# Performance work log

Measured on AMD Instinct MI355X. Metric: run time of the kernel, lower is better.

Reference implementation:

```python
import jax, jax.numpy as jnp
import numpy as np
import math

D_MODEL = 1024
NHEAD = 16
FACTOR = 5


def setup_inputs() -> dict:
    key = jax.random.key(0)
    kq, kk, kv = jax.random.split(key, 3)
    B, L = 4, 2048
    Q = jax.random.normal(kq, (B, L, D_MODEL), dtype=jnp.float32)
    K = jax.random.normal(kk, (B, L, D_MODEL), dtype=jnp.float32)
    V = jax.random.normal(kv, (B, L, D_MODEL), dtype=jnp.float32)
    return {"Q": Q, "K": K, "V": V}


def reference(Q, K, V):
    B, q_len, _ = Q.shape
    k_len = K.shape[1]
    head_dim = D_MODEL // NHEAD
    scale = 1.0 / math.sqrt(head_dim)

    # [B, H, L, Dh]
    Qh = Q.reshape(B, q_len, NHEAD, head_dim).transpose(0, 2, 1, 3)
    Kh = K.reshape(B, k_len, NHEAD, head_dim).transpose(0, 2, 1, 3)
    Vh = V.reshape(B, k_len, NHEAD, head_dim).transpose(0, 2, 1, 3)

    # Dense scores for KL-based query selection
    scores = jnp.einsum('bhqd,bhkd->bhqk', Qh, Kh) * scale
    logp = jax.nn.log_softmax(scores, axis=-1)
    probs = jnp.exp(logp)
    # KL(p || uniform) = sum p * (log p + log k_len)
    kl_div = jnp.sum(probs * (logp + jnp.log(jnp.float32(k_len))), axis=-1)  # [B,H,Q]

    top_u = min(int(FACTOR * math.log(q_len)), q_len)
    _, indices = jax.lax.top_k(kl_div, top_u)  # [B,H,U]

    # Gather selected queries
    Q_sparse = jnp.take_along_axis(Qh, indices[..., None], axis=2)  # [B,H,U,Dh]
    scores_sparse = jnp.einsum('bhud,bhkd->bhuk', Q_sparse, Kh) * scale
    attn_weights = jax.nn.softmax(scores_sparse, axis=-1)  # dropout p=0 (eval)
    output_sparse = jnp.einsum('bhuk,bhkd->bhud', attn_weights, Vh)

    # Scatter back into full-length output (non-selected queries are zero)
    b_idx = jnp.arange(B)[:, None, None]
    h_idx = jnp.arange(NHEAD)[None, :, None]
    output_full = jnp.zeros_like(Qh).at[b_idx, h_idx, indices].set(output_sparse)

    output = output_full.transpose(0, 2, 1, 3).reshape(B, q_len, D_MODEL)
    return output, attn_weights
```

## Files before the change

kernel.cpp:

```cpp
#include <hip/hip_runtime.h>
#include <math.h>

#define LQ 2048
#define DM 1024
#define NH 16
#define DH 64
#define UU 38
#define NBH 64
#define SCALE 0.125f

typedef _Float16 f16x8 __attribute__((ext_vector_type(8)));
typedef float f32x4 __attribute__((ext_vector_type(4)));
typedef float f32x2 __attribute__((ext_vector_type(2)));

#if __has_builtin(__builtin_amdgcn_exp2f)
#define EXP2F(x) __builtin_amdgcn_exp2f(x)
#else
#define EXP2F(x) exp2f(x)
#endif

#define GL2LDS16(gp, lp)                                           \
  __builtin_amdgcn_global_load_lds(                                \
      (const __attribute__((address_space(1))) void*)(gp),         \
      (__attribute__((address_space(3))) void*)(lp), 16, 0, 0)

#define F_OFF_SEL   4194304
#define F_OFF_L3    4204032
#define F_OFF_MASK  4213760
#define F_OFF_LPART 4344832
#define F_OFF_KSP   7146496
#define F_NEED      40700928ull

__global__ __launch_bounds__(256) void ksplit_kernel(const float* __restrict__ K,
                                                     _Float16* __restrict__ ksp) {
  int idx = blockIdx.x * 256 + threadIdx.x;
  int p = idx & 7;
  int k = (idx >> 3) & 63;
  int kc = (idx >> 9) & 31;
  int bh = idx >> 14;
  int b = bh >> 4, h = bh & 15;
  const float* src = K + ((size_t)(b * LQ + kc * 64 + k)) * DM + h * DH + (p ^ (k & 7)) * 8;
  float4 x0 = *(const float4*)src;
  float4 x1 = *(const float4*)(src + 4);
  f16x8 hi, lo;
#define KCV(i, xx) { float x_ = (xx); _Float16 hh = (_Float16)x_; hi[i] = hh; lo[i] = (_Float16)(x_ - (float)hh); }
  KCV(0, x0.x) KCV(1, x0.y) KCV(2, x0.z) KCV(3, x0.w)
  KCV(4, x1.x) KCV(5, x1.y) KCV(6, x1.z) KCV(7, x1.w)
#undef KCV
  _Float16* base = ksp + ((size_t)(bh * 32 + kc)) * 8192;
  *(f16x8*)(base + k * 64 + p * 8) = hi;
  *(f16x8*)(base + 4096 + k * 64 + p * 8) = lo;
}

__global__ __launch_bounds__(256) void kl_mfma2(const float* __restrict__ Q,
                                                const _Float16* __restrict__ ksp,
                                                double* __restrict__ lt) {
  int bh = blockIdx.x & 63;
  int qc = (blockIdx.x >> 6) & 15;
  int sp = blockIdx.x >> 10;
  int b = bh >> 4, h = bh & 15;
  int t = threadIdx.x;
  int lane = t & 63, w = t >> 6;
  int quad = lane >> 4, l15 = lane & 15;

  __shared__ __align__(16) _Float16 kbuf[8192];

  f16x8 ahi[2][2], alo[2][2];
  {
    const float* qrow = Q + ((size_t)(b * LQ + qc * 128)) * DM + h * DH;
#pragma unroll
    for (int qt = 0; qt < 2; ++qt)
#pragma unroll
      for (int c = 0; c < 2; ++c) {
        const float* p = qrow + (size_t)(w * 32 + qt * 16 + l15) * DM + c * 32 + quad * 8;
        float4 x0 = *(const float4*)p;
        float4 x1 = *(const float4*)(p + 4);
        f16x8 hi, lo;
#define QCV(i, xx) { float x_ = (xx); _Float16 hh = (_Float16)x_; hi[i] = hh; lo[i] = (_Float16)(x_ - (float)hh); }
        QCV(0, x0.x) QCV(1, x0.y) QCV(2, x0.z) QCV(3, x0.w)
        QCV(4, x1.x) QCV(5, x1.y) QCV(6, x1.z) QCV(7, x1.w)
#undef QCV
        ahi[qt][c] = hi;
        alo[qt][c] = lo;
      }
  }

  int bsw0 = quad ^ (l15 & 7);
  int bsw1 = (quad + 4) ^ (l15 & 7);
  const float C1 = 0.18033688011112042f;

  double l64[2][4], t64[2][4];
#pragma unroll
  for (int qt = 0; qt < 2; ++qt)
#pragma unroll
    for (int r = 0; r < 4; ++r) { l64[qt][r] = 0.0; t64[qt][r] = 0.0; }

  const _Float16* khiA = kbuf;
  const _Float16* kloA = kbuf + 2048;
  const _Float16* khiB = kbuf + 4096;
  const _Float16* kloB = kbuf + 6144;

  const char* gp = (const char*)(ksp + ((size_t)(bh * 32 + sp * 16)) * 8192) + t * 16;
  char* ldsA = (char*)kbuf + w * 1024;
  char* ldsB = (char*)kbuf + 8192 + w * 1024;

#define KLSTEP(KHI, KLO)                                                        \
  _Pragma("unroll")                                                             \
  for (int kt = 0; kt < 2; ++kt) {                                              \
    int key = kt * 16 + l15;                                                    \
    f16x8 bhi0 = *(const f16x8*)((KHI) + key * 64 + bsw0 * 8);                  \
    f16x8 bhi1 = *(const f16x8*)((KHI) + key * 64 + bsw1 * 8);                  \
    f16x8 blo0 = *(const f16x8*)((KLO) + key * 64 + bsw0 * 8);                  \
    f16x8 blo1 = *(const f16x8*)((KLO) + key * 64 + bsw1 * 8);                  \
    _Pragma("unroll")                                                           \
    for (int qt = 0; qt < 2; ++qt) {                                            \
      f32x4 cacc = {0.f, 0.f, 0.f, 0.f};                                        \
      cacc = __builtin_amdgcn_mfma_f32_16x16x32_f16(alo[qt][0], bhi0, cacc, 0, 0, 0); \
      cacc = __builtin_amdgcn_mfma_f32_16x16x32_f16(alo[qt][1], bhi1, cacc, 0, 0, 0); \
      cacc = __builtin_amdgcn_mfma_f32_16x16x32_f16(ahi[qt][0], blo0, cacc, 0, 0, 0); \
      cacc = __builtin_amdgcn_mfma_f32_16x16x32_f16(ahi[qt][1], blo1, cacc, 0, 0, 0); \
      cacc = __builtin_amdgcn_mfma_f32_16x16x32_f16(ahi[qt][0], bhi0, cacc, 0, 0, 0); \
      cacc = __builtin_amdgcn_mfma_f32_16x16x32_f16(ahi[qt][1], bhi1, cacc, 0, 0, 0); \
      _Pragma("unroll")                                                         \
      for (int rp = 0; rp < 2; ++rp) {                                          \
        f32x2 rr = { cacc[2 * rp], cacc[2 * rp + 1] };                          \
        f32x2 sc = rr * C1;                                   \
        f32x2 e  = { EXP2F(sc[0]), EXP2F(sc[1]) };                              \
        l32[qt][rp] += e;                                     \
        t32[qt][rp] += rr * e;                                \
      }                                                                         \
    }                                                                           \
  }

  GL2LDS16(gp, ldsA);
  GL2LDS16(gp + 8192, ldsA + 4096);
  __syncthreads();

  for (int j = 0; j < 16; ++j) {
    GL2LDS16(gp + 4096, ldsB);
    GL2LDS16(gp + 12288, ldsB + 4096);

    f32x2 l32[2][2], t32[2][2];
#pragma unroll
    for (int qt = 0; qt < 2; ++qt)
#pragma unroll
      for (int rp = 0; rp < 2; ++rp) {
        l32[qt][rp] = (f32x2){0.f, 0.f};
        t32[qt][rp] = (f32x2){0.f, 0.f};
      }

    KLSTEP(khiA, kloA)
    __syncthreads();

    if (j < 15) {
      gp += 16384;
      GL2LDS16(gp, ldsA);
      GL2LDS16(gp + 8192, ldsA + 4096);
    }

    KLSTEP(khiB, kloB)

#pragma unroll
    for (int qt = 0; qt < 2; ++qt)
#pragma unroll
      for (int rp = 0; rp < 2; ++rp)
#pragma unroll
        for (int c = 0; c < 2; ++c) {
          l64[qt][rp * 2 + c] += (double)l32[qt][rp][c];
          t64[qt][rp * 2 + c] += (double)t32[qt][rp][c];
        }
    __syncthreads();
  }
#undef KLSTEP

#pragma unroll
  for (int qt = 0; qt < 2; ++qt)
#pragma unroll
    for (int r = 0; r < 4; ++r) {
      double lv = l64[qt][r], tv = t64[qt][r];
#pragma unroll
      for (int m = 1; m < 16; m <<= 1) {
        lv += __shfl_xor(lv, m);
        tv += __shfl_xor(tv, m);
      }
      if (l15 == 0) {
        int qg = qc * 128 + w * 32 + qt * 16 + quad * 4 + r;
        double* dst = lt + ((size_t)(sp * 64 + bh) * LQ + qg) * 2;
        dst[0] = lv;
        dst[1] = tv;
      }
    }
}

__global__ __launch_bounds__(64) void topk2(const double* __restrict__ lt,
                                            int* __restrict__ idxout,
                                            signed char* __restrict__ selmask) {
  int bh = blockIdx.x;
  int lane = threadIdx.x;
  __shared__ double vals[LQ];
  const double logL = 7.624618986159398;

  double v1 = -INFINITY, v2 = -INFINITY, v3 = -INFINITY;
  int i1 = LQ, i2 = LQ, i3 = LQ;

  for (int j = 0; j < 32; ++j) {
    int i = j * 64 + lane;
    const double* p0 = lt + ((size_t)bh * LQ + i) * 2;
    const double* p1 = lt + ((size_t)(64 + bh) * LQ + i) * 2;
    double l = p0[0] + p1[0];
    double tt = p0[1] + p1[1];
    double v = 0.125 * (tt / l) - log(l) + logL;
    vals[i] = v;
    selmask[bh * LQ + i] = -1;
    if (v > v1)      { v3 = v2; i3 = i2; v2 = v1; i2 = i1; v1 = v; i1 = i; }
    else if (v > v2) { v3 = v2; i3 = i2; v2 = v;  i2 = i; }
    else if (v > v3) { v3 = v;  i3 = i; }
  }

  for (int u = 0; u < UU; ++u) {
    if (i1 == LQ) {
      v1 = v2 = v3 = -INFINITY;
      i1 = i2 = i3 = LQ;
      for (int j = 0; j < 32; ++j) {
        int i = j * 64 + lane;
        double v = vals[i];
        if (v > v1)      { v3 = v2; i3 = i2; v2 = v1; i2 = i1; v1 = v; i1 = i; }
        else if (v > v2) { v3 = v2; i3 = i2; v2 = v;  i2 = i; }
        else if (v > v3) { v3 = v;  i3 = i; }
      }
    }

    double gv = v1;
    int gi = i1;
#pragma unroll
    for (int m = 1; m < 64; m <<= 1) {
      double ov = __shfl_xor(gv, m);
      int oi = __shfl_xor(gi, m);
      if (ov > gv || (ov == gv && oi < gi)) { gv = ov; gi = oi; }
    }
    if (lane == 0) {
      idxout[bh * UU + u] = gi;
      selmask[bh * LQ + gi] = (signed char)u;
    }
    if ((gi & 63) == lane) {
      vals[gi] = -INFINITY;
      v1 = v2; i1 = i2;
      v2 = v3; i2 = i3;
      v3 = -INFINITY; i3 = LQ;
    }
  }
}

__global__ __launch_bounds__(256) void attn_w_mfma(const float* __restrict__ Q,
                                                   const _Float16* __restrict__ ksp,
                                                   const int* __restrict__ sel,
                                                   float* __restrict__ wout,
                                                   float* __restrict__ lpart) {
  int bh = blockIdx.x >> 4;
  int ks = blockIdx.x & 15;
  int b = bh >> 4, h = bh & 15;
  int t = threadIdx.x;
  int lane = t & 63, w = t >> 6;
  int quad = lane >> 4, l15 = lane & 15;

  __shared__ __align__(16) _Float16 kbuf[8192];
  __shared__ float els[48 * 132];
  __shared__ int sidx[UU];

  if (t < UU) sidx[t] = sel[bh * UU + t];
  __syncthreads();

  f16x8 ahi[3][2], alo[3][2];
#pragma unroll
  for (int qt = 0; qt < 3; ++qt) {
    int u = qt * 16 + l15;
    if (u > 37) u = 37;
    const float* qrow = Q + ((size_t)(b * LQ + sidx[u])) * DM + h * DH;
#pragma unroll
    for (int c = 0; c < 2; ++c) {
      const float* p = qrow + c * 32 + quad * 8;
      float4 x0 = *(const float4*)p;
      float4 x1 = *(const float4*)(p + 4);
      f16x8 hi, lo;
#define QCV(i, xx) { float x_ = (xx); _Float16 hh = (_Float16)x_; hi[i] = hh; lo[i] = (_Float16)(x_ - (float)hh); }
      QCV(0, x0.x) QCV(1, x0.y) QCV(2, x0.z) QCV(3, x0.w)
      QCV(4, x1.x) QCV(5, x1.y) QCV(6, x1.z) QCV(7, x1.w)
#undef QCV
      ahi[qt][c] = hi;
      alo[qt][c] = lo;
    }
  }

  int bsw0 = quad ^ (l15 & 7);
  int bsw1 = (quad + 4) ^ (l15 & 7);
  const float C1 = 0.18033688011112042f;
  const char* gch = (const char*)(ksp + ((size_t)(bh * 32 + ks * 2)) * 8192);
  _Float16* khi = kbuf;
  _Float16* klo = kbuf + 4096;

  for (int chunk = 0; chunk < 2; ++chunk) {
    __syncthreads();
    {
      const char* gs = gch + (size_t)chunk * 16384 + (size_t)t * 16;
      char* ls = (char*)kbuf + (size_t)(w * 64) * 16;
#pragma unroll
      for (int i = 0; i < 4; ++i)
        GL2LDS16(gs + i * 4096, ls + i * 4096);
    }
    __syncthreads();
    int key = w * 16 + l15;
    f16x8 bhi0 = *(const f16x8*)(khi + key * 64 + bsw0 * 8);
    f16x8 bhi1 = *(const f16x8*)(khi + key * 64 + bsw1 * 8);
    f16x8 blo0 = *(const f16x8*)(klo + key * 64 + bsw0 * 8);
    f16x8 blo1 = *(const f16x8*)(klo + key * 64 + bsw1 * 8);
#pragma unroll
    for (int qt = 0; qt < 3; ++qt) {
      f32x4 cacc = {0.f, 0.f, 0.f, 0.f};
      cacc = __builtin_amdgcn_mfma_f32_16x16x32_f16(alo[qt][0], bhi0, cacc, 0, 0, 0);
      cacc = __builtin_amdgcn_mfma_f32_16x16x32_f16(alo[qt][1], bhi1, cacc, 0, 0, 0);
      cacc = __builtin_amdgcn_mfma_f32_16x16x32_f16(ahi[qt][0], blo0, cacc, 0, 0, 0);
      cacc = __builtin_amdgcn_mfma_f32_16x16x32_f16(ahi[qt][1], blo1, cacc, 0, 0, 0);
      cacc = __builtin_amdgcn_mfma_f32_16x16x32_f16(ahi[qt][0], bhi0, cacc, 0, 0, 0);
      cacc = __builtin_amdgcn_mfma_f32_16x16x32_f16(ahi[qt][1], bhi1, cacc, 0, 0, 0);
#pragma unroll
      for (int r = 0; r < 4; ++r) {
        float e = EXP2F(cacc[r] * C1);
        els[(qt * 16 + quad * 4 + r) * 132 + chunk * 64 + w * 16 + l15] = e;
      }
    }
  }
  __syncthreads();

  for (int i = t; i < UU * 128; i += 256) {
    int u = i >> 7, k = i & 127;
    wout[((size_t)(bh * UU + u)) * LQ + ks * 128 + k] = els[u * 132 + k];
  }

#pragma unroll
  for (int p = 0; p < 10; ++p) {
    int u = w + 4 * p;
    if (u < UU) {
      float s = els[u * 132 + lane] + els[u * 132 + 64 + lane];
#pragma unroll
      for (int m = 1; m < 64; m <<= 1) s += __shfl_xor(s, m);
      if (lane == 0) lpart[(bh * 16 + ks) * UU + u] = s;
    }
  }
}

__global__ __launch_bounds__(256) void attn_pv2(const float* __restrict__ V,
                                                float* __restrict__ wout,
                                                const float* __restrict__ lpart,
                                                float* __restrict__ opart) {
  int bh = blockIdx.x >> 4;
  int ks = blockIdx.x & 15;
  int b = bh >> 4, h = bh & 15;
  int t = threadIdx.x;
  int d = t & 63, ug = t >> 6;

  __shared__ float ps[40 * 132];
  __shared__ float l3s[UU];

  if (t < UU) {
    float s = 0.f;
#pragma unroll
    for (int i = 0; i < 16; ++i) s += lpart[(bh * 16 + i) * UU + t];
    l3s[t] = 1.f / s;
  }
  for (int i = t; i < 2 * 132; i += 256) ps[UU * 132 + i] = 0.f;
  __syncthreads();

  for (int i = t; i < UU * 32; i += 256) {
    int u = i >> 5, d4 = i & 31;
    float r = l3s[u];
    float* wp = wout + ((size_t)(bh * UU + u)) * LQ + ks * 128 + d4 * 4;
    float4 v = *(const float4*)wp;
    v.x *= r; v.y *= r; v.z *= r; v.w *= r;
    *(float4*)(ps + u * 132 + d4 * 4) = v;
    *(float4*)wp = v;
  }
  __syncthreads();

  const float* vbase = V + ((size_t)(b * LQ + ks * 128)) * DM + h * DH + d;
  float o[10];
#pragma unroll
  for (int p = 0; p < 10; ++p) o[p] = 0.f;

  for (int j4 = 0; j4 < 128; j4 += 4) {
    float v0 = vbase[(size_t)(j4 + 0) * DM];
    float v1 = vbase[(size_t)(j4 + 1) * DM];
    float v2 = vbase[(size_t)(j4 + 2) * DM];
    float v3 = vbase[(size_t)(j4 + 3) * DM];
#pragma unroll
    for (int p = 0; p < 10; ++p) {
      float4 pw = *(const float4*)(ps + (ug + 4 * p) * 132 + j4);
      o[p] = fmaf(pw.x, v0, o[p]);
      o[p] = fmaf(pw.y, v1, o[p]);
      o[p] = fmaf(pw.z, v2, o[p]);
      o[p] = fmaf(pw.w, v3, o[p]);
    }
  }

#pragma unroll
  for (int p = 0; p < 10; ++p) {
    int u = ug + 4 * p;
    if (u < UU) opart[((size_t)((bh * 16 + ks) * UU + u)) * DH + d] = o[p];
  }
}

__global__ __launch_bounds__(256) void writeout_kernel(const signed char* __restrict__ selmask,
                                                       const float* __restrict__ opart,
                                                       float* __restrict__ out) {
  int i2 = blockIdx.x * 256 + threadIdx.x;
  int d = i2 & 63;
  int h = (i2 >> 6) & 15;
  int q = (i2 >> 10) & 2047;
  int b = i2 >> 21;
  int bh = b * 16 + h;
  int u = selmask[bh * LQ + q];
  float val = 0.f;
  if (u >= 0) {
    float s = 0.f;
#pragma unroll
    for (int p = 0; p < 16; ++p)
      s += opart[((size_t)((bh * 16 + p) * UU + u)) * DH + d];
    val = s;
  }
  out[i2] = val;
}

extern "C" void kernel_launch(void* const* d_in, const int* in_sizes, int n_in,
                              void* d_out, int out_size, void* d_ws, size_t ws_size,
                              hipStream_t stream) {
  (void)in_sizes; (void)n_in;
  if (ws_size < F_NEED) return;
  const float* Q = (const float*)d_in[0];
  const float* K = (const float*)d_in[1];
  const float* V = (const float*)d_in[2];
  float* out = (float*)d_out;
  float* wout = out + (size_t)4 * LQ * DM;
  char* ws = (char*)d_ws;

  double* lt = (double*)ws;
  int* sel = (int*)(ws + F_OFF_SEL);
  signed char* mask = (signed char*)(ws + F_OFF_MASK);
  float* lpart = (float*)(ws + F_OFF_LPART);
  _Float16* ksp = (_Float16*)(ws + F_OFF_KSP);
  float* opart = (float*)(ws + F_OFF_KSP);

  ksplit_kernel<<<4096, 256, 0, stream>>>(K, ksp);
  kl_mfma2<<<2048, 256, 0, stream>>>(Q, ksp, lt);
  topk2<<<NBH, 64, 0, stream>>>(lt, sel, mask);
  attn_w_mfma<<<NBH * 16, 256, 0, stream>>>(Q, ksp, sel, wout, lpart);
  attn_pv2<<<NBH * 16, 256, 0, stream>>>(V, wout, lpart, opart);
  writeout_kernel<<<(4 * LQ * DM) / 256, 256, 0, stream>>>(mask, opart, out);
}
```

Measured before the change: 344.2 us.

## Fuse attention weights with PV and reuse KL-pass softmax denominators

The top-k kernel now also saves the softmax denominator of each selected query, taken from the KL scoring pass, into a new small buffer. The attention-weight kernel uses it to normalise the exponentials directly and then runs the P·V product from shared memory in the same block. This removes the separate PV kernel, the partial row-sum reduction, and the read-modify-write of the full weight matrix in global memory. The per-block partial outputs are written over that block's own slice of the split-K workspace, which is safe only if each block alone reads that region. The weights now depend on denominators accumulated in the earlier pass, which could shift numerics slightly.

```diff
diff --git a/kernel.cpp b/kernel.cpp
--- a/kernel.cpp
+++ b/kernel.cpp
@@ -194,10 +194,12 @@
 
 __global__ __launch_bounds__(64) void topk2(const double* __restrict__ lt,
                                             int* __restrict__ idxout,
-                                            signed char* __restrict__ selmask) {
+                                            signed char* __restrict__ selmask,
+                                            float* __restrict__ l3out) {
   int bh = blockIdx.x;
   int lane = threadIdx.x;
   __shared__ double vals[LQ];
+  __shared__ float lsh[LQ];
   const double logL = 7.624618986159398;
 
   double v1 = -INFINITY, v2 = -INFINITY, v3 = -INFINITY;
@@ -211,6 +213,7 @@
     double tt = p0[1] + p1[1];
     double v = 0.125 * (tt / l) - log(l) + logL;
     vals[i] = v;
+    lsh[i] = (float)l;
     selmask[bh * LQ + i] = -1;
     if (v > v1)      { v3 = v2; i3 = i2; v2 = v1; i2 = i1; v1 = v; i1 = i; }
     else if (v > v2) { v3 = v2; i3 = i2; v2 = v;  i2 = i; }
@@ -243,6 +246,7 @@
       selmask[bh * LQ + gi] = (signed char)u;
     }
     if ((gi & 63) == lane) {
+      l3out[bh * UU + u] = lsh[gi];
       vals[gi] = -INFINITY;
       v1 = v2; i1 = i2;
       v2 = v3; i2 = i3;
@@ -251,11 +255,13 @@
   }
 }
 
-__global__ __launch_bounds__(256) void attn_w_mfma(const float* __restrict__ Q,
-                                                   const _Float16* __restrict__ ksp,
-                                                   const int* __restrict__ sel,
-                                                   float* __restrict__ wout,
-                                                   float* __restrict__ lpart) {
+__global__ __launch_bounds__(256) void attn_w_pv(const float* __restrict__ Q,
+                                                 const _Float16* __restrict__ ksp,
+                                                 const int* __restrict__ sel,
+                                                 const float* __restrict__ l3,
+                                                 const float* __restrict__ V,
+                                                 float* __restrict__ wout,
+                                                 float* __restrict__ kspf) {
   int bh = blockIdx.x >> 4;
   int ks = blockIdx.x & 15;
   int b = bh >> 4, h = bh & 15;
@@ -266,8 +272,10 @@
   __shared__ __align__(16) _Float16 kbuf[8192];
   __shared__ float els[48 * 132];
   __shared__ int sidx[UU];
+  __shared__ float l3i[48];
 
   if (t < UU) sidx[t] = sel[bh * UU + t];
+  if (t < 48) l3i[t] = (t < UU) ? 1.f / l3[bh * UU + t] : 0.f;
   __syncthreads();
 
   f16x8 ahi[3][2], alo[3][2];
@@ -324,8 +332,9 @@
       cacc = __builtin_amdgcn_mfma_f32_16x16x32_f16(ahi[qt][1], bhi1, cacc, 0, 0, 0);
 #pragma unroll
       for (int r = 0; r < 4; ++r) {
-        float e = EXP2F(cacc[r] * C1);
-        els[(qt * 16 + quad * 4 + r) * 132 + chunk * 64 + w * 16 + l15] = e;
+        int row = qt * 16 + quad * 4 + r;
+        float e = EXP2F(cacc[r] * C1) * l3i[row];
+        els[row * 132 + chunk * 64 + w * 16 + l15] = e;
       }
     }
   }
@@ -336,51 +345,7 @@
     wout[((size_t)(bh * UU + u)) * LQ + ks * 128 + k] = els[u * 132 + k];
   }
 
-#pragma unroll
-  for (int p = 0; p < 10; ++p) {
-    int u = w + 4 * p;
-    if (u < UU) {
-      float s = els[u * 132 + lane] + els[u * 132 + 64 + lane];
-#pragma unroll
-      for (int m = 1; m < 64; m <<= 1) s += __shfl_xor(s, m);
-      if (lane == 0) lpart[(bh * 16 + ks) * UU + u] = s;
-    }
-  }
-}
-
-__global__ __launch_bounds__(256) void attn_pv2(const float* __restrict__ V,
-                                                float* __restrict__ wout,
-                                                const float* __restrict__ lpart,
-                                                float* __restrict__ opart) {
-  int bh = blockIdx.x >> 4;
-  int ks = blockIdx.x & 15;
-  int b = bh >> 4, h = bh & 15;
-  int t = threadIdx.x;
   int d = t & 63, ug = t >> 6;
-
-  __shared__ float ps[40 * 132];
-  __shared__ float l3s[UU];
-
-  if (t < UU) {
-    float s = 0.f;
-#pragma unroll
-    for (int i = 0; i < 16; ++i) s += lpart[(bh * 16 + i) * UU + t];
-    l3s[t] = 1.f / s;
-  }
-  for (int i = t; i < 2 * 132; i += 256) ps[UU * 132 + i] = 0.f;
-  __syncthreads();
-
-  for (int i = t; i < UU * 32; i += 256) {
-    int u = i >> 5, d4 = i & 31;
-    float r = l3s[u];
-    float* wp = wout + ((size_t)(bh * UU + u)) * LQ + ks * 128 + d4 * 4;
-    float4 v = *(const float4*)wp;
-    v.x *= r; v.y *= r; v.z *= r; v.w *= r;
-    *(float4*)(ps + u * 132 + d4 * 4) = v;
-    *(float4*)wp = v;
-  }
-  __syncthreads();
-
   const float* vbase = V + ((size_t)(b * LQ + ks * 128)) * DM + h * DH + d;
   float o[10];
 #pragma unroll
@@ -393,7 +358,7 @@
     float v3 = vbase[(size_t)(j4 + 3) * DM];
 #pragma unroll
     for (int p = 0; p < 10; ++p) {
-      float4 pw = *(const float4*)(ps + (ug + 4 * p) * 132 + j4);
+      float4 pw = *(const float4*)(els + (ug + 4 * p) * 132 + j4);
       o[p] = fmaf(pw.x, v0, o[p]);
       o[p] = fmaf(pw.y, v1, o[p]);
       o[p] = fmaf(pw.z, v2, o[p]);
@@ -401,15 +366,16 @@
     }
   }
 
+  float* oslice = kspf + (size_t)(bh * 32 + ks * 2) * 4096;
 #pragma unroll
   for (int p = 0; p < 10; ++p) {
     int u = ug + 4 * p;
-    if (u < UU) opart[((size_t)((bh * 16 + ks) * UU + u)) * DH + d] = o[p];
+    if (u < UU) oslice[u * 64 + d] = o[p];
   }
 }
 
 __global__ __launch_bounds__(256) void writeout_kernel(const signed char* __restrict__ selmask,
-                                                       const float* __restrict__ opart,
+                                                       const float* __restrict__ kspf,
                                                        float* __restrict__ out) {
   int i2 = blockIdx.x * 256 + threadIdx.x;
   int d = i2 & 63;
@@ -420,10 +386,11 @@
   int u = selmask[bh * LQ + q];
   float val = 0.f;
   if (u >= 0) {
+    const float* base = kspf + (size_t)(bh * 32) * 4096 + u * 64 + d;
     float s = 0.f;
 #pragma unroll
     for (int p = 0; p < 16; ++p)
-      s += opart[((size_t)((bh * 16 + p) * UU + u)) * DH + d];
+      s += base[(size_t)(p * 2) * 4096];
     val = s;
   }
   out[i2] = val;
@@ -443,15 +410,14 @@
 
   double* lt = (double*)ws;
   int* sel = (int*)(ws + F_OFF_SEL);
+  float* l3 = (float*)(ws + F_OFF_L3);
   signed char* mask = (signed char*)(ws + F_OFF_MASK);
-  float* lpart = (float*)(ws + F_OFF_LPART);
   _Float16* ksp = (_Float16*)(ws + F_OFF_KSP);
-  float* opart = (float*)(ws + F_OFF_KSP);
+  float* kspf = (float*)(ws + F_OFF_KSP);
 
   ksplit_kernel<<<4096, 256, 0, stream>>>(K, ksp);
   kl_mfma2<<<2048, 256, 0, stream>>>(Q, ksp, lt);
-  topk2<<<NBH, 64, 0, stream>>>(lt, sel, mask);
-  attn_w_mfma<<<NBH * 16, 256, 0, stream>>>(Q, ksp, sel, wout, lpart);
-  attn_pv2<<<NBH * 16, 256, 0, stream>>>(V, wout, lpart, opart);
-  writeout_kernel<<<(4 * LQ * DM) / 256, 256, 0, stream>>>(mask, opart, out);
-}
+  topk2<<<NBH, 64, 0, stream>>>(lt, sel, mask, l3);
+  attn_w_pv<<<NBH * 16, 256, 0, stream>>>(Q, ksp, sel, l3, V, wout, kspf);
+  writeout_kernel<<<(4 * LQ * DM) / 256, 256, 0, stream>>>(mask, kspf, out);
+}
```

After: 345.0 us. No clear change (+0.2%).
